# Performance work log

Hardware: AMD Instinct MI355X
Metric: run time of the kernel (lower is better)

Reference implementation:

```python
import jax, jax.numpy as jnp
import numpy as np

D_MODEL = 96
D_STATE = 16
D_INNER = 192   # expand * d_model
DT_RANK = 6     # ceil(96/16)
D_DEPTH_OUT = 1024  # (64/2)*(64/2)
BATCH, HH, WW = 2, 64, 64


def silu(v):
    return v * jax.nn.sigmoid(v)


def setup_inputs() -> dict:
    key = jax.random.key(0)
    ks = jax.random.split(key, 10)
    f = jnp.float32
    x = jax.random.normal(ks[0], (BATCH, HH, WW, D_MODEL), f)
    in_proj_w = jax.random.normal(ks[1], (2 * D_INNER, D_MODEL), f) * 0.02
    conv2d_w = jax.random.normal(ks[2], (D_INNER, 1, 3, 3), f) * 0.1  # depthwise, groups=D_INNER
    conv2d_b = jnp.zeros((D_INNER,), f)
    depth_conv_w = jax.random.normal(ks[3], (D_INNER, 1, 3, 3), f) * 0.1  # depthwise, stride 2
    depth_conv_b = jnp.zeros((D_INNER,), f)
    depth_fc_w = jax.random.normal(ks[4], (D_INNER, D_DEPTH_OUT), f) * 0.02
    depth_fc_b = jnp.zeros((D_INNER,), f)
    x_proj_w = jax.random.normal(ks[5], (DT_RANK + 2 * D_STATE, D_INNER), f) * 0.02
    dt_init_std = DT_RANK ** (-0.5)
    dt_projs_w = jax.random.uniform(ks[6], (D_INNER, DT_RANK), f, -dt_init_std, dt_init_std)
    # inverse-softplus of dt ~ U(log 1e-3, log 0.1)
    dt = jnp.exp(jax.random.uniform(ks[7], (D_INNER,), f) * (np.log(0.1) - np.log(0.001)) + np.log(0.001))
    dt = jnp.clip(dt, 1e-4, None)
    dt_projs_b = dt + jnp.log(-jnp.expm1(-dt))
    A_logs = jnp.log(jnp.tile(jnp.arange(1, D_STATE + 1, dtype=f)[None, :], (D_INNER, 1)))
    Ds = jnp.ones((D_INNER,), f)
    out_norm_w = jnp.ones((D_INNER,), f)
    out_norm_b = jnp.zeros((D_INNER,), f)
    out_proj_w = jax.random.normal(ks[8], (D_MODEL, D_INNER), f) * 0.02
    return dict(x=x, in_proj_w=in_proj_w, conv2d_w=conv2d_w, conv2d_b=conv2d_b,
                depth_conv_w=depth_conv_w, depth_conv_b=depth_conv_b,
                depth_fc_w=depth_fc_w, depth_fc_b=depth_fc_b, x_proj_w=x_proj_w,
                dt_projs_w=dt_projs_w, dt_projs_b=dt_projs_b, A_logs=A_logs, Ds=Ds,
                out_norm_w=out_norm_w, out_norm_b=out_norm_b, out_proj_w=out_proj_w)


def _selective_scan(u, delta, A, Bm, Cm, D, delta_bias):
    # u, delta: [B, D, L]; A: [D, N]; Bm, Cm: [B, N, L]; D: [D]; delta_bias: [D]
    delta = jax.nn.softplus(delta + delta_bias[None, :, None])
    dA = jnp.exp(jnp.einsum('bdl,dn->lbdn', delta, A))          # [L,B,D,N]
    dBu = jnp.einsum('bdl,bnl,bdl->lbdn', delta, Bm, u)          # [L,B,D,N]
    Ct = jnp.transpose(Cm, (2, 0, 1))                            # [L,B,N]
    h0 = jnp.zeros(dA.shape[1:], u.dtype)

    def step(h, inp):
        a, b, c = inp
        h = a * h + b                                            # S6 recurrence
        return h, jnp.einsum('bdn,bn->bd', h, c)

    _, ys = jax.lax.scan(step, h0, (dA, dBu, Ct))                # ys: [L,B,D]
    y = jnp.transpose(ys, (1, 2, 0))                             # [B,D,L]
    return y + D[None, :, None] * u


def _forward(x, in_proj_w, conv2d_w, conv2d_b, depth_conv_w, depth_conv_b,
             depth_fc_w, depth_fc_b, x_proj_w, dt_projs_w, dt_projs_b,
             A_logs, Ds, out_norm_w, out_norm_b, out_proj_w):
    B, H, W, _ = x.shape
    Di, N, R = D_INNER, D_STATE, DT_RANK
    dn = ('NCHW', 'OIHW', 'NCHW')
    xz = x @ in_proj_w.T
    x1, z = jnp.split(xz, 2, axis=-1)
    xc = jnp.transpose(x1, (0, 3, 1, 2))                         # [B,Di,H,W]
    xc = jax.lax.conv_general_dilated(xc, conv2d_w, (1, 1), [(1, 1), (1, 1)],
                                      dimension_numbers=dn, feature_group_count=Di)
    xc = silu(xc + conv2d_b[None, :, None, None])
    dxc = jax.lax.conv_general_dilated(xc, depth_conv_w, (2, 2), [(1, 1), (1, 1)],
                                       dimension_numbers=dn, feature_group_count=Di)
    dxc = dxc + depth_conv_b[None, :, None, None]                # [B,Di,H/2,W/2]
    dx = dxc.reshape(B, Di, -1)                                  # [B,Di,1024]
    dx = dx @ depth_fc_w.T + depth_fc_b                          # [B,Di,Di]
    dx = silu(jnp.transpose(dx, (0, 2, 1)))                      # [B,Di,CC], CC=Di
    L = H * W
    CC = dx.shape[-1]
    xs = jnp.concatenate([dx, xc.reshape(B, Di, L)], axis=-1)    # mode='head': [B,Di,LL]
    x_dbl = jnp.einsum('bdl,cd->bcl', xs, x_proj_w)
    dts, Bm, Cm = x_dbl[:, :R], x_dbl[:, R:R + N], x_dbl[:, R + N:]
    dts = jnp.einsum('brl,dr->bdl', dts, dt_projs_w)
    A = -jnp.exp(A_logs)
    y = _selective_scan(xs, dts, A, Bm, Cm, Ds, dt_projs_b)
    y = y[..., CC:]                                              # drop depth tokens (head mode)
    y = jnp.transpose(y, (0, 2, 1)).reshape(B, H, W, Di)
    mu = jnp.mean(y, axis=-1, keepdims=True)
    var = jnp.var(y, axis=-1, keepdims=True)
    y = (y - mu) * jax.lax.rsqrt(var + 1e-5) * out_norm_w + out_norm_b
    y = y * silu(z)
    return y @ out_proj_w.T


def reference(x, in_proj_w, conv2d_w, conv2d_b, depth_conv_w, depth_conv_b,
              depth_fc_w, depth_fc_b, x_proj_w, dt_projs_w, dt_projs_b,
              A_logs, Ds, out_norm_w, out_norm_b, out_proj_w):
    return _forward(x, in_proj_w, conv2d_w, conv2d_b, depth_conv_w, depth_conv_b,
                    depth_fc_w, depth_fc_b, x_proj_w, dt_projs_w, dt_projs_b,
                    A_logs, Ds, out_norm_w, out_norm_b, out_proj_w)
```

## Files before the change

### kernel.cpp

```cpp
#include <hip/hip_runtime.h>
#include <hip/hip_bf16.h>

typedef __hip_bfloat16 bf16;

#define BATCH 2
#define DM 96
#define DI 192
#define LSP 4096
#define LD 192
#define LTOT 4288
#define NST 16
#define RK 6
#define DFC 1024
#define CLEN 64
#define NCH 67
#define XR 16
#define NG  (BATCH * DI * NST)

__device__ __forceinline__ float b2f(bf16 v) { return __bfloat162float(v); }
__device__ __forceinline__ float silu_f(float x) { return x / (1.f + __expf(-x)); }
__device__ __forceinline__ float softplus_f(float x) { return x > 20.f ? x : log1pf(__expf(x)); }

__device__ __forceinline__ int is_f32(const void* alog) {
    return ((const unsigned int*)alog)[0] == 0u;
}
__device__ __forceinline__ float LDI(const void* p, int i, int f32m) {
    return f32m ? ((const float*)p)[i] : __bfloat162float(((const bf16*)p)[i]);
}
__device__ __forceinline__ void unpack2(unsigned int u, float* o) {
    o[0] = __uint_as_float(u << 16);
    o[1] = __uint_as_float(u & 0xffff0000u);
}

__global__ __launch_bounds__(768) void k_inproj(const void* __restrict__ x, const void* __restrict__ ipw,
                                                const void* __restrict__ alog,
                                                float* __restrict__ x1, float* __restrict__ z) {
    __shared__ uint4 sxr[384];
    const int f32m = is_f32(alog);
    int t = threadIdx.x;
    int col = t >> 1;
    int kh = t & 1;
    int row0 = blockIdx.x * 16;
    float wr[48];
    if (f32m) {
        const float4* wp = (const float4*)((const float*)ipw + col * 96 + kh * 48);
        #pragma unroll
        for (int i = 0; i < 12; i++) {
            float4 v = wp[i];
            wr[4*i] = v.x; wr[4*i+1] = v.y; wr[4*i+2] = v.z; wr[4*i+3] = v.w;
        }
        if (t < 384) sxr[t] = ((const uint4*)((const float*)x + row0 * 96))[t];
        __syncthreads();
        for (int r = 0; r < 16; r++) {
            const uint4* xr = &sxr[r * 24 + kh * 12];
            float acc = 0.f;
            #pragma unroll
            for (int i = 0; i < 12; i++) {
                uint4 u = xr[i];
                acc += __uint_as_float(u.x) * wr[4*i]   + __uint_as_float(u.y) * wr[4*i+1]
                     + __uint_as_float(u.z) * wr[4*i+2] + __uint_as_float(u.w) * wr[4*i+3];
            }
            acc += __shfl_xor(acc, 1);
            if (kh == 0) {
                int row = row0 + r;
                if (col < DI) x1[row * DI + col] = acc;
                else          z[row * DI + (col - DI)] = acc;
            }
        }
    } else {
        const uint4* wp = (const uint4*)((const bf16*)ipw + col * 96 + kh * 48);
        #pragma unroll
        for (int i = 0; i < 6; i++) {
            uint4 v = wp[i];
            unpack2(v.x, &wr[8*i]);   unpack2(v.y, &wr[8*i+2]);
            unpack2(v.z, &wr[8*i+4]); unpack2(v.w, &wr[8*i+6]);
        }
        if (t < 192) sxr[t] = ((const uint4*)((const bf16*)x + row0 * 96))[t];
        __syncthreads();
        for (int r = 0; r < 16; r++) {
            const uint4* xr = &sxr[r * 12 + kh * 6];
            float acc = 0.f;
            #pragma unroll
            for (int i = 0; i < 6; i++) {
                uint4 xv = xr[i];
                float xf8[8];
                unpack2(xv.x, &xf8[0]); unpack2(xv.y, &xf8[2]);
                unpack2(xv.z, &xf8[4]); unpack2(xv.w, &xf8[6]);
                #pragma unroll
                for (int j = 0; j < 8; j++) acc += xf8[j] * wr[8*i + j];
            }
            acc += __shfl_xor(acc, 1);
            if (kh == 0) {
                int row = row0 + r;
                if (col < DI) x1[row * DI + col] = acc;
                else          z[row * DI + (col - DI)] = acc;
            }
        }
    }
}

__global__ __launch_bounds__(192) void k_conv1(const float* __restrict__ x1, const void* __restrict__ cw,
                                               const void* __restrict__ cb, float* __restrict__ xs,
                                               const void* __restrict__ alog) {
    const int f32m = is_f32(alog);
    int d = threadIdx.x;
    int blk = blockIdx.x;
    int b = blk >> 9;
    int rest = blk & 511;
    int h = rest >> 3, w0 = (rest & 7) * 8;
    float wgt[9];
    #pragma unroll
    for (int i = 0; i < 9; i++) wgt[i] = LDI(cw, d * 9 + i, f32m);
    float bias = LDI(cb, d, f32m);
    float val[3][10];
    #pragma unroll
    for (int dh = 0; dh < 3; dh++) {
        int hh = h + dh - 1;
        #pragma unroll
        for (int j = 0; j < 10; j++) {
            int ww = w0 + j - 1;
            val[dh][j] = ((unsigned)hh < 64u && (unsigned)ww < 64u)
                       ? x1[((b << 12) + (hh << 6) + ww) * DI + d] : 0.f;
        }
    }
    #pragma unroll
    for (int i = 0; i < 8; i++) {
        float acc = bias;
        #pragma unroll
        for (int dh = 0; dh < 3; dh++)
            #pragma unroll
            for (int dw = 0; dw < 3; dw++)
                acc += val[dh][i + dw] * wgt[dh * 3 + dw];
        xs[(b * LTOT + LD + (h << 6) + w0 + i) * DI + d] = silu_f(acc);
    }
}

__global__ __launch_bounds__(192) void k_conv2(const float* __restrict__ xs, const void* __restrict__ dw,
                                               const void* __restrict__ db, float* __restrict__ dxc,
                                               const void* __restrict__ alog) {
    const int f32m = is_f32(alog);
    int d = threadIdx.x;
    int blk = blockIdx.x;
    int b = blk >> 10, lp = blk & 1023;
    int hp = lp >> 5, wp = lp & 31;
    float acc = LDI(db, d, f32m);
    #pragma unroll
    for (int dh = 0; dh < 3; dh++) {
        int h = 2 * hp + dh - 1;
        if ((unsigned)h >= 64u) continue;
        #pragma unroll
        for (int dw_ = 0; dw_ < 3; dw_++) {
            int w_ = 2 * wp + dw_ - 1;
            if ((unsigned)w_ >= 64u) continue;
            acc += xs[(b * LTOT + LD + (h << 6) + w_) * DI + d] * LDI(dw, d * 9 + dh * 3 + dw_, f32m);
        }
    }
    dxc[(b * DFC + lp) * DI + d] = acc;
}

__global__ __launch_bounds__(192) void k_dfc(const float* __restrict__ dxc, const void* __restrict__ fw,
                                             float* __restrict__ part, const void* __restrict__ alog) {
    __shared__ float sfw[4 * 128];
    const int f32m = is_f32(alog);
    int t = threadIdx.x;
    int blk = blockIdx.x;
    int p = blk / 96;
    int rem = blk - p * 96;
    int b   = rem / 48;
    int ch0 = (rem % 48) * 4;
    int k0  = p * 128;
    for (int idx = t; idx < 4 * 128; idx += 192)
        sfw[idx] = LDI(fw, (ch0 + (idx >> 7)) * DFC + k0 + (idx & 127), f32m);
    __syncthreads();
    float a0 = 0.f, a1 = 0.f, a2 = 0.f, a3 = 0.f;
    #pragma unroll 8
    for (int k = 0; k < 128; k++) {
        float dv = dxc[(b * DFC + k0 + k) * DI + t];
        a0 += dv * sfw[k];
        a1 += dv * sfw[128 + k];
        a2 += dv * sfw[256 + k];
        a3 += dv * sfw[384 + k];
    }
    int ob = ((p * 2 + b) * 192 + t) * DI + ch0;
    *(float4*)&part[ob] = make_float4(a0, a1, a2, a3);
}

__global__ __launch_bounds__(256) void k_xdbl(const float* __restrict__ xs_r, float* __restrict__ xs_w,
                                              const float* __restrict__ part, const void* __restrict__ fb,
                                              const void* __restrict__ xpw,
                                              float* __restrict__ BCb, float* __restrict__ dts,
                                              const void* __restrict__ alog) {
    __shared__ float sw[38 * 196];
    __shared__ float srow[XR][196];
    const int f32m = is_f32(alog);
    int t = threadIdx.x;
    for (int c = t >> 3; c < 38; c += 32) {
        int seg = (t & 7) * 24;
        for (int k = seg; k < seg + 24; k++) sw[c * 196 + k] = LDI(xpw, c * DI + k, f32m);
    }
    int row0 = blockIdx.x * XR;
    int bb = row0 >= LTOT ? 1 : 0;
    int depth = (row0 - bb * LTOT) < LD;
    for (int idx = t; idx < XR * DI; idx += 256) {
        int row = idx / DI, k = idx - row * DI;
        int grow = row0 + row;
        float v;
        if (depth) {
            int tok = grow - bb * LTOT;
            int o = (bb * 192 + tok) * DI + k;
            v = 0.f;
            #pragma unroll
            for (int p = 0; p < 8; p++) v += part[o + p * 73728];
            v = silu_f(v + LDI(fb, k, f32m));
            xs_w[grow * DI + k] = v;
        } else {
            v = xs_r[grow * DI + k];
        }
        srow[row][k] = v;
    }
    __syncthreads();
    int r = t & 15, cg = t >> 4;
    float a0 = 0.f, a1 = 0.f, a2 = 0.f;
    const float4* w0 = (const float4*)&sw[cg * 196];
    const float4* w1 = (const float4*)&sw[(cg + 16) * 196];
    const float4* w2 = (const float4*)&sw[(cg < 6 ? cg + 32 : cg) * 196];
    const float4* xr = (const float4*)&srow[r][0];
    #pragma unroll 4
    for (int k = 0; k < 48; k++) {
        float4 xv = xr[k], v0 = w0[k], v1 = w1[k], v2 = w2[k];
        a0 += xv.x * v0.x + xv.y * v0.y + xv.z * v0.z + xv.w * v0.w;
        a1 += xv.x * v1.x + xv.y * v1.y + xv.z * v1.z + xv.w * v1.w;
        a2 += xv.x * v2.x + xv.y * v2.y + xv.z * v2.z + xv.w * v2.w;
    }
    int grow = row0 + r;
    if (cg < 6) dts[grow * 6 + cg] = a0;
    else        BCb[grow * 32 + (cg - 6)] = a0;
    BCb[grow * 32 + (cg + 10)] = a1;
    if (cg < 6) BCb[grow * 32 + (cg + 26)] = a2;
}

__device__ __forceinline__ void delta_block(const float* sdts, const float* sdwb, float* sdel, int t) {
    int e = t * 4;
    int i = e >> 4, dl = e & 15;
    #pragma unroll
    for (int q = 0; q < 4; q++) {
        int dlq = dl + q;
        float dv = sdwb[96 + dlq];
        #pragma unroll
        for (int r2 = 0; r2 < RK; r2++) dv += sdts[i * RK + r2] * sdwb[dlq * RK + r2];
        sdel[e + q] = softplus_f(dv);
    }
}

__global__ __launch_bounds__(256) void k_scan1(const float* __restrict__ dts, const float* __restrict__ xs,
                                               const float* __restrict__ BCb, const void* __restrict__ dtw,
                                               const void* __restrict__ dtb, const void* __restrict__ alog,
                                               float2* __restrict__ AH) {
    __shared__ float su[CLEN * 16];
    __shared__ float sB[CLEN * 16];
    __shared__ float sdel[CLEN * 16];
    __shared__ float sdts[CLEN * RK];
    __shared__ float sdwb[112];
    const int f32m = is_f32(alog);
    int t = threadIdx.x;
    int beta = blockIdx.x;
    int b = beta / (12 * NCH);
    int rem = beta - b * (12 * NCH);
    int dblk = rem / NCH, ch = rem - dblk * NCH;
    int d0 = dblk * 16, l0 = ch * CLEN;
    int bL = b * LTOT;
    {
        int e = t * 4;
        int i = e >> 4, dd = e & 15;
        *(float4*)&su[e] = *(const float4*)&xs[(bL + l0 + i) * DI + d0 + dd];
        *(float4*)&sB[e] = *(const float4*)&BCb[(bL + l0 + i) * 32 + dd];
    }
    for (int idx = t; idx < CLEN * RK; idx += 256) sdts[idx] = dts[(bL + l0) * RK + idx];
    if (t < 96)            sdwb[t] = LDI(dtw, (d0 + t / 6) * RK + (t % 6), f32m);
    else if (t < 112)      sdwb[t] = LDI(dtb, d0 + (t - 96), f32m);
    __syncthreads();
    delta_block(sdts, sdwb, sdel, t);
    __syncthreads();
    int dloc = t >> 4, n = t & 15;
    int d = d0 + dloc;
    float A = -__expf(LDI(alog, d * NST + n, f32m));
    float h = 0.f, ap = 1.f;
    #pragma unroll 4
    for (int i = 0; i < CLEN; i++) {
        float dt = sdel[(i << 4) | dloc];
        float u  = su[(i << 4) | dloc];
        float Bv = sB[(i << 4) | n];
        float a = __expf(dt * A);
        h = a * h + dt * Bv * u;
        ap *= a;
    }
    int g = ((b * DI + d) * NST) + n;
    AH[ch * NG + g] = make_float2(ap, h);
}

__global__ __launch_bounds__(256) void k_scan3(const float* __restrict__ dts, const float* __restrict__ xs,
                                               const float* __restrict__ BCb, const void* __restrict__ dtw,
                                               const void* __restrict__ dtb, const void* __restrict__ alog,
                                               const void* __restrict__ Dsv, const float2* __restrict__ AH,
                                               float* __restrict__ y) {
    __shared__ float su[CLEN * 16];
    __shared__ float sbc[CLEN * 32];
    __shared__ float sdel[CLEN * 16];
    __shared__ float sdts[CLEN * RK];
    __shared__ float sdwb[112];
    const int f32m = is_f32(alog);
    int t = threadIdx.x;
    int beta = blockIdx.x;
    int b = beta / (12 * NCH);
    int rem = beta - b * (12 * NCH);
    int dblk = rem / NCH, ch = rem - dblk * NCH;
    int d0 = dblk * 16, l0 = ch * CLEN;
    int bL = b * LTOT;
    {
        int e = t * 4;
        int i = e >> 4, dd = e & 15;
        *(float4*)&su[e] = *(const float4*)&xs[(bL + l0 + i) * DI + d0 + dd];
    }
    #pragma unroll
    for (int q = 0; q < 2; q++) {
        int e = (t + q * 256) * 4;
        int i = e >> 5, c = e & 31;
        *(float4*)&sbc[e] = *(const float4*)&BCb[(bL + l0 + i) * 32 + c];
    }
    for (int idx = t; idx < CLEN * RK; idx += 256) sdts[idx] = dts[(bL + l0) * RK + idx];
    if (t < 96)            sdwb[t] = LDI(dtw, (d0 + t / 6) * RK + (t % 6), f32m);
    else if (t < 112)      sdwb[t] = LDI(dtb, d0 + (t - 96), f32m);
    int dloc = t >> 4, n = t & 15;
    int d = d0 + dloc;
    int g = ((b * DI + d) * NST) + n;
    float h = 0.f;
    for (int c = 0; c < ch; c++) {
        float2 v = AH[c * NG + g];
        h = v.x * h + v.y;
    }
    __syncthreads();
    delta_block(sdts, sdwb, sdel, t);
    __syncthreads();
    float A = -__expf(LDI(alog, d * NST + n, f32m));
    float Dv = LDI(Dsv, d, f32m);
    for (int i = 0; i < CLEN; i++) {
        float dt = sdel[(i << 4) | dloc];
        float u  = su[(i << 4) | dloc];
        float Bv = sbc[(i << 5) | n];
        float Cv = sbc[(i << 5) | 16 | n];
        float a = __expf(dt * A);
        h = a * h + dt * Bv * u;
        float yv = h * Cv;
        #pragma unroll
        for (int m = 8; m; m >>= 1) yv += __shfl_xor(yv, m, 16);
        int l = l0 + i;
        if (n == 0 && l >= LD) y[(b * LSP + (l - LD)) * DI + d] = yv + Dv * u;
    }
}

__global__ __launch_bounds__(384) void k_out(const float* __restrict__ y, const float* __restrict__ z,
                                             const void* __restrict__ nw, const void* __restrict__ nb,
                                             const void* __restrict__ opw, void* __restrict__ out,
                                             const void* __restrict__ alog) {
    __shared__ float sg[2][DI];
    __shared__ float sred[2][2][3];
    const int f32m = is_f32(alog);
    int t = threadIdx.x;
    int m = t >> 2, kh = t & 3;
    float wr[48];
    if (f32m) {
        const float4* wp = (const float4*)((const float*)opw + m * DI + kh * 48);
        #pragma unroll
        for (int i = 0; i < 12; i++) {
            float4 v = wp[i];
            wr[4*i] = v.x; wr[4*i+1] = v.y; wr[4*i+2] = v.z; wr[4*i+3] = v.w;
        }
    } else {
        const uint4* wp = (const uint4*)((const bf16*)opw + m * DI + kh * 48);
        #pragma unroll
        for (int i = 0; i < 6; i++) {
            uint4 v = wp[i];
            unpack2(v.x, &wr[8*i]);   unpack2(v.y, &wr[8*i+2]);
            unpack2(v.z, &wr[8*i+4]); unpack2(v.w, &wr[8*i+6]);
        }
    }
    float nwv = 0.f, nbv = 0.f;
    if (t < DI) { nwv = LDI(nw, t, f32m); nbv = LDI(nb, t, f32m); }
    int wv_ = t >> 6;
    int row0 = blockIdx.x * 16;
    for (int pr = 0; pr < 8; pr++) {
        int r0 = row0 + pr * 2, r1 = r0 + 1;
        float y0 = 0.f, z0 = 0.f, y1 = 0.f, z1 = 0.f;
        if (t < DI) {
            y0 = y[r0 * DI + t]; z0 = z[r0 * DI + t];
            y1 = y[r1 * DI + t]; z1 = z[r1 * DI + t];
            float s0 = y0, q0 = y0 * y0, s1 = y1, q1 = y1 * y1;
            #pragma unroll
            for (int off = 32; off; off >>= 1) {
                s0 += __shfl_xor(s0, off); q0 += __shfl_xor(q0, off);
                s1 += __shfl_xor(s1, off); q1 += __shfl_xor(q1, off);
            }
            if ((t & 63) == 0) {
                sred[0][0][wv_] = s0; sred[0][1][wv_] = q0;
                sred[1][0][wv_] = s1; sred[1][1][wv_] = q1;
            }
        }
        __syncthreads();
        if (t < DI) {
            float S0  = sred[0][0][0] + sred[0][0][1] + sred[0][0][2];
            float Q0  = sred[0][1][0] + sred[0][1][1] + sred[0][1][2];
            float S1  = sred[1][0][0] + sred[1][0][1] + sred[1][0][2];
            float Q1  = sred[1][1][0] + sred[1][1][1] + sred[1][1][2];
            float mu0 = S0 * (1.f / 192.f), var0 = Q0 * (1.f / 192.f) - mu0 * mu0;
            float mu1 = S1 * (1.f / 192.f), var1 = Q1 * (1.f / 192.f) - mu1 * mu1;
            float g0 = (y0 - mu0) * rsqrtf(var0 + 1e-5f) * nwv + nbv;
            g0 *= z0 / (1.f + __expf(-z0));
            float g1 = (y1 - mu1) * rsqrtf(var1 + 1e-5f) * nwv + nbv;
            g1 *= z1 / (1.f + __expf(-z1));
            sg[0][t] = g0;
            sg[1][t] = g1;
        }
        __syncthreads();
        const float* g0p = &sg[0][kh * 48];
        const float* g1p = &sg[1][kh * 48];
        float a0 = 0.f, a1 = 0.f;
        #pragma unroll
        for (int j = 0; j < 48; j++) {
            a0 += g0p[j] * wr[j];
            a1 += g1p[j] * wr[j];
        }
        a0 += __shfl_xor(a0, 1); a0 += __shfl_xor(a0, 2);
        a1 += __shfl_xor(a1, 1); a1 += __shfl_xor(a1, 2);
        if (kh == 0) {
            if (f32m) {
                ((float*)out)[r0 * DM + m] = a0;
                ((float*)out)[r1 * DM + m] = a1;
            } else {
                ((bf16*)out)[r0 * DM + m] = __float2bfloat16(a0);
                ((bf16*)out)[r1 * DM + m] = __float2bfloat16(a1);
            }
        }
    }
}

extern "C" void kernel_launch(void* const* d_in, const int* in_sizes, int n_in,
                              void* d_out, int out_size, void* d_ws, size_t ws_size,
                              hipStream_t stream) {
    (void)in_sizes; (void)n_in; (void)out_size; (void)ws_size;
    const void* x    = d_in[0];
    const void* ipw  = d_in[1];
    const void* c1w  = d_in[2];
    const void* c1b  = d_in[3];
    const void* c2w  = d_in[4];
    const void* c2b  = d_in[5];
    const void* fcw  = d_in[6];
    const void* fcb  = d_in[7];
    const void* xpw  = d_in[8];
    const void* dtw  = d_in[9];
    const void* dtb  = d_in[10];
    const void* alog = d_in[11];
    const void* Dsv  = d_in[12];
    const void* nw   = d_in[13];
    const void* nb   = d_in[14];
    const void* opw  = d_in[15];

    float* ws  = (float*)d_ws;
    float* x1  = ws;
    float* z   = x1  + BATCH * LSP * DI;
    float* xs  = z   + BATCH * LSP * DI;
    float* dxc = xs  + BATCH * LTOT * DI;
    float* BCb = dxc + BATCH * DFC * DI;
    float* dts = BCb + BATCH * LTOT * 32;
    float2* AH = (float2*)(dts + BATCH * LTOT * RK);
    float* part = x1;
    float* y    = x1;

    k_inproj<<<dim3(512), dim3(768), 0, stream>>>(x, ipw, alog, x1, z);
    k_conv1 <<<dim3(1024), dim3(DI), 0, stream>>>(x1, c1w, c1b, xs, alog);
    k_conv2 <<<dim3(BATCH * DFC), dim3(DI), 0, stream>>>(xs, c2w, c2b, dxc, alog);
    k_dfc   <<<dim3(768), dim3(DI), 0, stream>>>(dxc, fcw, part, alog);
    k_xdbl  <<<dim3(536), dim3(256), 0, stream>>>(xs, xs, part, fcb, xpw, BCb, dts, alog);
    k_scan1 <<<dim3(BATCH * 12 * NCH), dim3(256), 0, stream>>>(dts, xs, BCb, dtw, dtb, alog, AH);
    k_scan3 <<<dim3(BATCH * 12 * NCH), dim3(256), 0, stream>>>(dts, xs, BCb, dtw, dtb, alog, Dsv, AH, y);
    k_out   <<<dim3(512), dim3(384), 0, stream>>>(y, z, nw, nb, opw, d_out, alog);
}
```

Measured before the change: 225.5 us.

## Halve scan chunk length, skip depth-token chunks in output pass, stage y in LDS

```diff
diff --git a/kernel.cpp b/kernel.cpp
--- a/kernel.cpp
+++ b/kernel.cpp
@@ -12,8 +12,9 @@
 #define NST 16
 #define RK 6
 #define DFC 1024
-#define CLEN 64
-#define NCH 67
+#define CLEN 32
+#define NCH 134
+#define SCH 128
 #define XR 16
 #define NG  (BATCH * DI * NST)
 
@@ -240,6 +241,7 @@
 }
 
 __device__ __forceinline__ void delta_block(const float* sdts, const float* sdwb, float* sdel, int t) {
+    if (t >= 128) return;
     int e = t * 4;
     int i = e >> 4, dl = e & 15;
     #pragma unroll
@@ -269,13 +271,13 @@
     int dblk = rem / NCH, ch = rem - dblk * NCH;
     int d0 = dblk * 16, l0 = ch * CLEN;
     int bL = b * LTOT;
-    {
+    if (t < 128) {
         int e = t * 4;
         int i = e >> 4, dd = e & 15;
         *(float4*)&su[e] = *(const float4*)&xs[(bL + l0 + i) * DI + d0 + dd];
         *(float4*)&sB[e] = *(const float4*)&BCb[(bL + l0 + i) * 32 + dd];
     }
-    for (int idx = t; idx < CLEN * RK; idx += 256) sdts[idx] = dts[(bL + l0) * RK + idx];
+    if (t < CLEN * RK)     sdts[t] = dts[(bL + l0) * RK + t];
     if (t < 96)            sdwb[t] = LDI(dtw, (d0 + t / 6) * RK + (t % 6), f32m);
     else if (t < 112)      sdwb[t] = LDI(dtb, d0 + (t - 96), f32m);
     __syncthreads();
@@ -306,28 +308,28 @@
     __shared__ float su[CLEN * 16];
     __shared__ float sbc[CLEN * 32];
     __shared__ float sdel[CLEN * 16];
+    __shared__ float sy[CLEN * 16];
     __shared__ float sdts[CLEN * RK];
     __shared__ float sdwb[112];
     const int f32m = is_f32(alog);
     int t = threadIdx.x;
     int beta = blockIdx.x;
-    int b = beta / (12 * NCH);
-    int rem = beta - b * (12 * NCH);
-    int dblk = rem / NCH, ch = rem - dblk * NCH;
+    int b = beta / (12 * SCH);
+    int rem = beta - b * (12 * SCH);
+    int dblk = rem / SCH, ch = (rem - dblk * SCH) + 6;
     int d0 = dblk * 16, l0 = ch * CLEN;
     int bL = b * LTOT;
-    {
+    if (t < 128) {
         int e = t * 4;
         int i = e >> 4, dd = e & 15;
         *(float4*)&su[e] = *(const float4*)&xs[(bL + l0 + i) * DI + d0 + dd];
     }
-    #pragma unroll
-    for (int q = 0; q < 2; q++) {
-        int e = (t + q * 256) * 4;
+    {
+        int e = t * 4;
         int i = e >> 5, c = e & 31;
         *(float4*)&sbc[e] = *(const float4*)&BCb[(bL + l0 + i) * 32 + c];
     }
-    for (int idx = t; idx < CLEN * RK; idx += 256) sdts[idx] = dts[(bL + l0) * RK + idx];
+    if (t < CLEN * RK)     sdts[t] = dts[(bL + l0) * RK + t];
     if (t < 96)            sdwb[t] = LDI(dtw, (d0 + t / 6) * RK + (t % 6), f32m);
     else if (t < 112)      sdwb[t] = LDI(dtb, d0 + (t - 96), f32m);
     int dloc = t >> 4, n = t & 15;
@@ -353,8 +355,13 @@
         float yv = h * Cv;
         #pragma unroll
         for (int m = 8; m; m >>= 1) yv += __shfl_xor(yv, m, 16);
-        int l = l0 + i;
-        if (n == 0 && l >= LD) y[(b * LSP + (l - LD)) * DI + d] = yv + Dv * u;
+        if (n == 0) sy[(i << 4) | dloc] = yv + Dv * u;
+    }
+    __syncthreads();
+    if (t < 128) {
+        int e = t * 4;
+        int i = e >> 4, dd = e & 15;
+        *(float4*)&y[(b * LSP + l0 + i - LD) * DI + d0 + dd] = *(const float4*)&sy[e];
     }
 }
 
@@ -481,6 +488,6 @@
     k_dfc   <<<dim3(768), dim3(DI), 0, stream>>>(dxc, fcw, part, alog);
     k_xdbl  <<<dim3(536), dim3(256), 0, stream>>>(xs, xs, part, fcb, xpw, BCb, dts, alog);
     k_scan1 <<<dim3(BATCH * 12 * NCH), dim3(256), 0, stream>>>(dts, xs, BCb, dtw, dtb, alog, AH);
-    k_scan3 <<<dim3(BATCH * 12 * NCH), dim3(256), 0, stream>>>(dts, xs, BCb, dtw, dtb, alog, Dsv, AH, y);
+    k_scan3 <<<dim3(BATCH * 12 * SCH), dim3(256), 0, stream>>>(dts, xs, BCb, dtw, dtb, alog, Dsv, AH, y);
     k_out   <<<dim3(512), dim3(384), 0, stream>>>(y, z, nw, nb, opw, d_out, alog);
 }
```

After: 272.1 us. +20.7%, slower.
